# Kernel tuning notes

Hardware: AMD Instinct MI355X
Metric: run time of the kernel (lower is better)

## Reference

```python
import jax, jax.numpy as jnp
import numpy as np

N = 50000   # nodes
E = 800000  # edges
D = 64      # num_filters == hidden_channels
NG = 5      # num_gaussians (edge_attr width, unused by forward math)
NEG_SLOPE = 0.2


def setup_inputs() -> dict:
    key = jax.random.key(0)
    ks = jax.random.split(key, 16)
    s = 1.0 / np.sqrt(D)
    return {
        "x": jax.random.normal(ks[0], (N, D), dtype=jnp.float32),
        "edge_index": jax.random.randint(ks[1], (2, E), 0, N, dtype=jnp.int64),
        "edge_weight": jax.random.uniform(ks[2], (E,), dtype=jnp.float32),
        "edge_attr": jax.random.normal(ks[3], (E, NG), dtype=jnp.float32),
        "W0": jax.random.normal(ks[4], (D, D), dtype=jnp.float32) * s,
        "b0": jnp.zeros((D,), dtype=jnp.float32),
        "W1": jax.random.normal(ks[5], (D, D), dtype=jnp.float32) * s,
        "as1": jax.random.normal(ks[6], (D,), dtype=jnp.float32) * s,
        "ad1": jax.random.normal(ks[7], (D,), dtype=jnp.float32) * s,
        "b1": jnp.zeros((D,), dtype=jnp.float32),
        "W2": jax.random.normal(ks[8], (D, D), dtype=jnp.float32) * s,
        "as2": jax.random.normal(ks[9], (D,), dtype=jnp.float32) * s,
        "ad2": jax.random.normal(ks[10], (D,), dtype=jnp.float32) * s,
        "b2": jnp.zeros((D,), dtype=jnp.float32),
    }


def gat_layer(h, src, dst, W, a_src, a_dst, b):
    # PyG GATConv, heads=1, add_self_loops=False
    hx = h @ W  # [N, D]
    # per-node attention logits, gathered per edge (edge j->i: src=j, dst=i)
    alpha = (hx * a_src).sum(-1)[src] + (hx * a_dst).sum(-1)[dst]  # [E]
    alpha = jax.nn.leaky_relu(alpha, NEG_SLOPE)
    # segment softmax grouped by destination node
    m = jax.ops.segment_max(alpha, dst, num_segments=N)
    e = jnp.exp(alpha - m[dst])
    s = jax.ops.segment_sum(e, dst, num_segments=N)
    p = e / s[dst]  # [E]
    # scatter-add weighted source features
    out = jax.ops.segment_sum(hx[src] * p[:, None], dst, num_segments=N)
    return out + b


def reference(x, edge_index, edge_weight, edge_attr,
              W0, b0, W1, as1, ad1, b1, W2, as2, ad2, b2):
    # edge_weight / edge_attr are accepted but unused, as in the torch module
    src, dst = edge_index[0], edge_index[1]
    out = jax.nn.relu(x @ W0 + b0)
    out = out + jax.nn.relu(gat_layer(out, src, dst, W1, as1, ad1, b1))
    out = out + jax.nn.relu(gat_layer(out, src, dst, W2, as2, ad2, b2))
    return out
```

## Files before the change

### kernel.cpp

```cpp
#include <hip/hip_runtime.h>

#define DD 64
#define NEG_SLOPE 0.2f
#define HS 68
#define CAP 64
#define BSH 8
#define BN  256
#define NBMAX 256
#define NBLK 256
#define CAPB 6144
#define STAGE_CAP 6144
#define AMM_NODES 32
#define CWS 65

__device__ __forceinline__ unsigned short f2bf(float f)
{
    unsigned u = __float_as_uint(f);
    u += 0x7FFFu + ((u >> 16) & 1u);
    return (unsigned short)(u >> 16);
}
__device__ __forceinline__ float bf2f(unsigned short b)
{
    return __uint_as_float(((unsigned)b) << 16);
}

__device__ __forceinline__ int wave_incl_scan(int v, int lane)
{
#pragma unroll
    for (int off = 1; off < 64; off <<= 1) {
        int t = __shfl_up(v, off);
        if (lane >= off) v += t;
    }
    return v;
}

__device__ __forceinline__ void group_aggregate(
    const ushort4* __restrict__ hx, const int* __restrict__ col,
    const float* __restrict__ sarr, float adi, int beg, int deg, int fl,
    uint2* __restrict__ cw, float4& acc, float& s)
{
    s = 0.f;
    acc = float4{0.f, 0.f, 0.f, 0.f};

#define GATH(P) { float wv = __uint_as_float((P).y);                          \
                  ushort4 uu = hx[(P).x * 16 + fl];                           \
                  acc.x += wv * bf2f(uu.x); acc.y += wv * bf2f(uu.y);         \
                  acc.z += wv * bf2f(uu.z); acc.w += wv * bf2f(uu.w); }

    if (deg <= CAP) {
        int c0 = 0, c1 = 0, c2 = 0, c3 = 0;
        float w0 = 0.f, w1 = 0.f, w2 = 0.f, w3 = 0.f;
        if (fl < deg)      { c0 = col[beg + fl];      float a = sarr[c0] + adi; a = a > 0.f ? a : NEG_SLOPE * a; w0 = __expf(a); }
        if (fl + 16 < deg) { c1 = col[beg + fl + 16]; float a = sarr[c1] + adi; a = a > 0.f ? a : NEG_SLOPE * a; w1 = __expf(a); }
        if (fl + 32 < deg) { c2 = col[beg + fl + 32]; float a = sarr[c2] + adi; a = a > 0.f ? a : NEG_SLOPE * a; w2 = __expf(a); }
        if (fl + 48 < deg) { c3 = col[beg + fl + 48]; float a = sarr[c3] + adi; a = a > 0.f ? a : NEG_SLOPE * a; w3 = __expf(a); }
        s = (w0 + w1) + (w2 + w3);

        int degR = (deg + 7) & ~7;
        if (fl < degR)      { uint2 e; e.x = (unsigned)c0; e.y = __float_as_uint(w0); cw[fl] = e; }
        if (fl + 16 < degR) { uint2 e; e.x = (unsigned)c1; e.y = __float_as_uint(w1); cw[fl + 16] = e; }
        if (fl + 32 < degR) { uint2 e; e.x = (unsigned)c2; e.y = __float_as_uint(w2); cw[fl + 32] = e; }
        if (fl + 48 < degR) { uint2 e; e.x = (unsigned)c3; e.y = __float_as_uint(w3); cw[fl + 48] = e; }

        for (int i = 0; i < degR; i += 8) {
            uint2 p0 = cw[i],     p1 = cw[i + 1], p2 = cw[i + 2], p3 = cw[i + 3];
            uint2 p4 = cw[i + 4], p5 = cw[i + 5], p6 = cw[i + 6], p7 = cw[i + 7];
            GATH(p0); GATH(p1); GATH(p2); GATH(p3);
            GATH(p4); GATH(p5); GATH(p6); GATH(p7);
        }
    } else {
        for (int base = 0; base < deg; base += 16) {
            int i = base + fl;
            uint2 e; e.x = 0u; e.y = 0u;
            if (i < deg) {
                int c = col[beg + i];
                float a = sarr[c] + adi;
                a = a > 0.f ? a : NEG_SLOPE * a;
                float wv = __expf(a);
                e.x = (unsigned)c; e.y = __float_as_uint(wv);
                s += wv;
            }
            cw[fl] = e;
#pragma unroll
            for (int j = 0; j < 16; j += 8) {
                uint2 p0 = cw[j],     p1 = cw[j + 1], p2 = cw[j + 2], p3 = cw[j + 3];
                uint2 p4 = cw[j + 4], p5 = cw[j + 5], p6 = cw[j + 6], p7 = cw[j + 7];
                GATH(p0); GATH(p1); GATH(p2); GATH(p3);
                GATH(p4); GATH(p5); GATH(p6); GATH(p7);
            }
        }
    }
#pragma unroll
    for (int off = 8; off; off >>= 1) s += __shfl_xor(s, off);
#undef GATH
}

__global__ __launch_bounds__(512) void scatter_mm(
    const int4* __restrict__ dst4, const int4* __restrict__ src4,
    const int* __restrict__ dst, const int* __restrict__ src,
    int* __restrict__ gcur, int* __restrict__ ebuf,
    int NB, int E4, int E, int C4,
    const float* __restrict__ x, const float* __restrict__ W0,
    const float* __restrict__ b0, const float* __restrict__ W1,
    const float* __restrict__ a_src, const float* __restrict__ a_dst,
    float* __restrict__ h, ushort4* __restrict__ hxb4,
    float* __restrict__ sarr, float* __restrict__ darr, int n)
{
    __shared__ float smem[DD * DD + DD * HS];
    int tid = threadIdx.x;

    if (blockIdx.x < NBLK) {
        int* lh   = (int*)smem;
        int* lcur = lh + NBMAX;
        int k = blockIdx.x;
        for (int i = tid; i < NB; i += 512) lh[i] = 0;
        __syncthreads();
        int i0 = k * C4, i1 = min(i0 + C4, E4);
        for (int i = i0 + tid; i < i1; i += 512) {
            int4 d = dst4[i];
            atomicAdd(&lh[d.x >> BSH], 1);
            atomicAdd(&lh[d.y >> BSH], 1);
            atomicAdd(&lh[d.z >> BSH], 1);
            atomicAdd(&lh[d.w >> BSH], 1);
        }
        if (k == NBLK - 1) {
            for (int e = E4 * 4 + tid; e < E; e += 512)
                atomicAdd(&lh[dst[e] >> BSH], 1);
        }
        __syncthreads();
        for (int b = tid; b < NB; b += 512) {
            int c = lh[b];
            lcur[b] = b * CAPB + (c ? atomicAdd(&gcur[b], c) : 0);
        }
        __syncthreads();
        for (int i = i0 + tid; i < i1; i += 512) {
            int4 d = dst4[i];
            int4 s = src4[i];
            int b, p;
            b = d.x >> BSH; p = atomicAdd(&lcur[b], 1);
            if (p < b * CAPB + CAPB) ebuf[p] = ((d.x & (BN - 1)) << 24) | s.x;
            b = d.y >> BSH; p = atomicAdd(&lcur[b], 1);
            if (p < b * CAPB + CAPB) ebuf[p] = ((d.y & (BN - 1)) << 24) | s.y;
            b = d.z >> BSH; p = atomicAdd(&lcur[b], 1);
            if (p < b * CAPB + CAPB) ebuf[p] = ((d.z & (BN - 1)) << 24) | s.z;
            b = d.w >> BSH; p = atomicAdd(&lcur[b], 1);
            if (p < b * CAPB + CAPB) ebuf[p] = ((d.w & (BN - 1)) << 24) | s.w;
        }
        if (k == NBLK - 1) {
            for (int e = E4 * 4 + tid; e < E; e += 512) {
                int d = dst[e];
                int b = d >> BSH;
                int p = atomicAdd(&lcur[b], 1);
                if (p < b * CAPB + CAPB)
                    ebuf[p] = ((d & (BN - 1)) << 24) | src[e];
            }
        }
        return;
    }

    float* Wsh = smem;
    float* Hsh = smem + DD * DD;
    int fg = tid & 15, ng = tid >> 4;
    int tile0 = (blockIdx.x - NBLK) * 64;

    for (int i = tid * 4; i < DD * DD; i += 2048)
        *(float4*)&Wsh[i] = *(const float4*)&W0[i];
    for (int p = 0; p < 2; ++p) {
        int nl = p * 32 + ng, gn = tile0 + nl;
        if (gn < n)
            *(float4*)&Hsh[nl * HS + 4 * fg] = *(const float4*)&x[gn * DD + 4 * fg];
    }
    __syncthreads();

    float4 acc[2];
#pragma unroll
    for (int j = 0; j < 2; ++j) acc[j] = float4{0.f, 0.f, 0.f, 0.f};
#pragma unroll 8
    for (int k = 0; k < DD; ++k) {
        float4 w4 = *(float4*)&Wsh[k * DD + 4 * fg];
#pragma unroll
        for (int j = 0; j < 2; ++j) {
            float hv = Hsh[(2 * ng + j) * HS + k];
            acc[j].x += hv * w4.x; acc[j].y += hv * w4.y;
            acc[j].z += hv * w4.z; acc[j].w += hv * w4.w;
        }
    }

    float4 b4 = *(const float4*)&b0[4 * fg];
    float4 o[2];
#pragma unroll
    for (int j = 0; j < 2; ++j) {
        o[j].x = fmaxf(acc[j].x + b4.x, 0.f);
        o[j].y = fmaxf(acc[j].y + b4.y, 0.f);
        o[j].z = fmaxf(acc[j].z + b4.z, 0.f);
        o[j].w = fmaxf(acc[j].w + b4.w, 0.f);
        int gn = tile0 + 2 * ng + j;
        if (gn < n) *(float4*)&h[gn * DD + 4 * fg] = o[j];
    }
    __syncthreads();

#pragma unroll
    for (int j = 0; j < 2; ++j)
        *(float4*)&Hsh[(2 * ng + j) * HS + 4 * fg] = o[j];
    for (int i = tid * 4; i < DD * DD; i += 2048)
        *(float4*)&Wsh[i] = *(const float4*)&W1[i];
    __syncthreads();

#pragma unroll
    for (int j = 0; j < 2; ++j) acc[j] = float4{0.f, 0.f, 0.f, 0.f};
#pragma unroll 8
    for (int k = 0; k < DD; ++k) {
        float4 w4 = *(float4*)&Wsh[k * DD + 4 * fg];
#pragma unroll
        for (int j = 0; j < 2; ++j) {
            float hv = Hsh[(2 * ng + j) * HS + k];
            acc[j].x += hv * w4.x; acc[j].y += hv * w4.y;
            acc[j].z += hv * w4.z; acc[j].w += hv * w4.w;
        }
    }

    float4 as4 = *(const float4*)&a_src[4 * fg];
    float4 ad4 = *(const float4*)&a_dst[4 * fg];
#pragma unroll
    for (int j = 0; j < 2; ++j) {
        int gn = tile0 + 2 * ng + j;
        if (gn < n) {
            ushort4 hb;
            hb.x = f2bf(acc[j].x); hb.y = f2bf(acc[j].y);
            hb.z = f2bf(acc[j].z); hb.w = f2bf(acc[j].w);
            hxb4[gn * 16 + fg] = hb;
        }
        float ps = acc[j].x * as4.x + acc[j].y * as4.y + acc[j].z * as4.z + acc[j].w * as4.w;
        float pd = acc[j].x * ad4.x + acc[j].y * ad4.y + acc[j].z * ad4.z + acc[j].w * ad4.w;
#pragma unroll
        for (int off = 8; off; off >>= 1) {
            ps += __shfl_xor(ps, off);
            pd += __shfl_xor(pd, off);
        }
        if (fg == 0 && gn < n) { sarr[gn] = ps; darr[gn] = pd; }
    }
}

__global__ __launch_bounds__(512) void group_build(
    const int* __restrict__ ebuf, const int* __restrict__ gcur,
    int* __restrict__ row_beg, int* __restrict__ degarr,
    int* __restrict__ col, int N)
{
    __shared__ int lcnt[BN];
    __shared__ int loff[BN];
    __shared__ int lcur[BN];
    __shared__ int wsum[4];
    __shared__ int stage[STAGE_CAP];
    int b = blockIdx.x, tid = threadIdx.x;
    int e0 = b * CAPB;
    int total = min(gcur[b], CAPB);
    int e1 = e0 + total;
    if (tid < BN) { lcnt[tid] = 0; lcur[tid] = 0; }
    __syncthreads();
    for (int e = e0 + tid; e < e1; e += 512)
        atomicAdd(&lcnt[((unsigned)ebuf[e]) >> 24], 1);
    __syncthreads();
    int lane = tid & 63, w = tid >> 6;
    int v = (tid < BN) ? lcnt[tid] : 0;
    int incl = wave_incl_scan(v, lane);
    if (tid < BN && lane == 63) wsum[w] = incl;
    __syncthreads();
    if (tid < BN) {
        int wo = 0;
        for (int i = 0; i < w; ++i) wo += wsum[i];
        int excl = wo + incl - v;
        loff[tid] = excl;
        int node = b * BN + tid;
        if (node < N) { row_beg[node] = e0 + excl; degarr[node] = v; }
    }
    __syncthreads();
    for (int e = e0 + tid; e < e1; e += 512) {
        int p = ebuf[e];
        int dl = ((unsigned)p) >> 24;
        int r = atomicAdd(&lcur[dl], 1);
        stage[loff[dl] + r] = p & 0xFFFFFF;
    }
    __syncthreads();
    for (int i = tid; i < total; i += 512)
        col[e0 + i] = stage[i];
}

__global__ __launch_bounds__(512) void agg_mm(
    const ushort4* __restrict__ hxA, const int* __restrict__ row_beg,
    const int* __restrict__ degarr, const int* __restrict__ col,
    const float* __restrict__ sA, const float* __restrict__ dA,
    const float* __restrict__ bias,
    float* __restrict__ h, const float* __restrict__ W,
    const float* __restrict__ a_src, const float* __restrict__ a_dst,
    ushort4* __restrict__ hxB, float* __restrict__ sB, float* __restrict__ dB,
    int n)
{
    __shared__ float Wsh[DD * DD];
    __shared__ uint2 cwbuf[AMM_NODES][CWS];
    float* Hsh = (float*)&cwbuf[0][0];

    int tid = threadIdx.x;
    int w = tid >> 6, lane = tid & 63, grp = lane >> 4, fl = lane & 15;
    int nl = 4 * w + grp;
    int tile0 = blockIdx.x * AMM_NODES;
    int v = tile0 + nl;
    bool alive = v < n;

    for (int i = tid * 4; i < DD * DD; i += 2048)
        *(float4*)&Wsh[i] = *(const float4*)&W[i];

    int beg = 0, deg = 0;
    float adi = 0.f;
    if (alive) {
        beg = row_beg[v];
        deg = degarr[v];
        adi = dA[v];
    }

    float4 acc; float s;
    group_aggregate(hxA, col, sA, adi, beg, deg, fl, &cwbuf[nl][0], acc, s);

    float4 resid = float4{0.f, 0.f, 0.f, 0.f};
    {
        float inv = (s > 0.f) ? 1.f / s : 0.f;
        float4 b4 = ((const float4*)bias)[fl];
        float4 o;
        o.x = fmaxf(acc.x * inv + b4.x, 0.f);
        o.y = fmaxf(acc.y * inv + b4.y, 0.f);
        o.z = fmaxf(acc.z * inv + b4.z, 0.f);
        o.w = fmaxf(acc.w * inv + b4.w, 0.f);
        if (alive) {
            float4* hp = (float4*)&h[v * DD + 4 * fl];
            float4 cur = *hp;
            cur.x += o.x; cur.y += o.y; cur.z += o.z; cur.w += o.w;
            *hp = cur;
            resid = cur;
        }
    }
    __syncthreads();
    *(float4*)&Hsh[nl * HS + 4 * fl] = resid;
    __syncthreads();

    int nl2 = tid >> 4;
    int fg = tid & 15;
    float4 acc2 = float4{0.f, 0.f, 0.f, 0.f};
#pragma unroll 8
    for (int k = 0; k < DD; ++k) {
        float4 w4 = *(float4*)&Wsh[k * DD + 4 * fg];
        float hv = Hsh[nl2 * HS + k];
        acc2.x += hv * w4.x; acc2.y += hv * w4.y;
        acc2.z += hv * w4.z; acc2.w += hv * w4.w;
    }
    int gn = tile0 + nl2;
    float4 as4 = *(const float4*)&a_src[4 * fg];
    float4 ad4 = *(const float4*)&a_dst[4 * fg];
    if (gn < n) {
        ushort4 hb;
        hb.x = f2bf(acc2.x); hb.y = f2bf(acc2.y);
        hb.z = f2bf(acc2.z); hb.w = f2bf(acc2.w);
        hxB[gn * 16 + fg] = hb;
    }
    float ps = acc2.x * as4.x + acc2.y * as4.y + acc2.z * as4.z + acc2.w * as4.w;
    float pd = acc2.x * ad4.x + acc2.y * ad4.y + acc2.z * ad4.z + acc2.w * ad4.w;
#pragma unroll
    for (int off = 8; off; off >>= 1) {
        ps += __shfl_xor(ps, off);
        pd += __shfl_xor(pd, off);
    }
    if (fg == 0 && gn < n) { sB[gn] = ps; dB[gn] = pd; }
}

__global__ __launch_bounds__(512) void aggregate(
    const ushort4* __restrict__ hxb4, const int* __restrict__ row_beg,
    const int* __restrict__ degarr, const int* __restrict__ col,
    const float* __restrict__ sarr, const float* __restrict__ darr,
    const float* __restrict__ bias, float* __restrict__ h, int n)
{
    __shared__ uint2 cwbuf[AMM_NODES][CWS];
    int tid = threadIdx.x;
    int w = tid >> 6, lane = tid & 63, grp = lane >> 4, fl = lane & 15;
    int nl = 4 * w + grp;
    int v = blockIdx.x * AMM_NODES + nl;
    bool alive = v < n;

    int beg = 0, deg = 0;
    float adi = 0.f;
    if (alive) {
        beg = row_beg[v];
        deg = degarr[v];
        adi = darr[v];
    }

    float4 acc; float s;
    group_aggregate(hxb4, col, sarr, adi, beg, deg, fl, &cwbuf[nl][0], acc, s);

    if (alive) {
        float inv = (s > 0.f) ? 1.f / s : 0.f;
        float4 b4 = ((const float4*)bias)[fl];
        float4 o;
        o.x = fmaxf(acc.x * inv + b4.x, 0.f);
        o.y = fmaxf(acc.y * inv + b4.y, 0.f);
        o.z = fmaxf(acc.z * inv + b4.z, 0.f);
        o.w = fmaxf(acc.w * inv + b4.w, 0.f);
        float4* hp = (float4*)&h[v * DD + 4 * fl];
        float4 cur = *hp;
        cur.x += o.x; cur.y += o.y; cur.z += o.z; cur.w += o.w;
        *hp = cur;
    }
}

extern "C" void kernel_launch(void* const* d_in, const int* in_sizes, int n_in,
                              void* d_out, int out_size, void* d_ws, size_t ws_size,
                              hipStream_t stream)
{
    const float* x  = (const float*)d_in[0];
    const int*   ei = (const int*)d_in[1];
    const float* W0 = (const float*)d_in[4];
    const float* b0 = (const float*)d_in[5];
    const float* W1 = (const float*)d_in[6];
    const float* as1= (const float*)d_in[7];
    const float* ad1= (const float*)d_in[8];
    const float* b1 = (const float*)d_in[9];
    const float* W2 = (const float*)d_in[10];
    const float* as2= (const float*)d_in[11];
    const float* ad2= (const float*)d_in[12];
    const float* b2 = (const float*)d_in[13];

    int N = in_sizes[0] / DD;
    int E = in_sizes[1] / 2;
    int E4 = E >> 2;
    int C4 = (E4 + NBLK - 1) / NBLK;
    int NB = (N + BN - 1) >> BSH;
    float* h = (float*)d_out;

    ushort4* hxA  = (ushort4*)d_ws;
    ushort4* hxB  = hxA + (size_t)N * 16;
    float* sA     = (float*)(hxB + (size_t)N * 16);
    float* dA     = sA + N;
    float* sB     = dA + N;
    float* dB     = sB + N;
    int*   row_beg= (int*)(dB + N);
    int*   degarr = row_beg + N;
    int*   gcur   = degarr + N;
    int*   ebuf   = gcur + NB;
    int*   colb   = ebuf + (size_t)NB * CAPB;

    const int* src = ei;
    const int* dst = ei + E;
    const int4* dst4 = (const int4*)dst;
    const int4* src4 = (const int4*)src;

    int tiles   = (N + 63) / 64;
    int ntiles  = (N + AMM_NODES - 1) / AMM_NODES;

    hipMemsetAsync(gcur, 0, NB * sizeof(int), stream);
    scatter_mm<<<NBLK + tiles, 512, 0, stream>>>(
        dst4, src4, dst, src, gcur, ebuf, NB, E4, E, C4,
        x, W0, b0, W1, as1, ad1, h, hxA, sA, dA, N);
    group_build<<<NB, 512, 0, stream>>>(ebuf, gcur, row_beg, degarr, colb, N);
    agg_mm<<<ntiles, 512, 0, stream>>>(hxA, row_beg, degarr, colb, sA, dA, b1,
                                       h, W2, as2, ad2, hxB, sB, dB, N);
    aggregate<<<ntiles, 512, 0, stream>>>(hxB, row_beg, degarr, colb,
                                          sB, dB, b2, h, N);
}
```

Measured before the change: 178.4 us.

## Fuse group_build into scatter_mm via per-bucket completion counters and late claiming

Removes the separate group_build launch. Each scatter block bumps a per-bucket counter with release semantics once its edges are written. Every block, at its end, claims any bucket whose counter shows all scatter blocks are done and builds that bucket's CSR segment in shared memory. This saves a kernel launch and lets CSR building overlap with the trailing matmul tiles. The cost is extra atomics and a smaller shared stage aliased onto smem, and buckets may be unevenly assigned to whichever blocks finish late.

```diff
diff --git a/kernel.cpp b/kernel.cpp
--- a/kernel.cpp
+++ b/kernel.cpp
@@ -95,10 +95,52 @@
 #undef GATH
 }
 
-__global__ __launch_bounds__(512) void scatter_mm(
+__device__ __forceinline__ void build_bucket(
+    int b, const int* __restrict__ ebuf, const int* __restrict__ gcur,
+    int* __restrict__ row_beg, int* __restrict__ degarr, int* __restrict__ col,
+    int N, int* stage, int* lcnt, int* loff, int* lcur, int* wsum)
+{
+    int tid = threadIdx.x;
+    int e0 = b * CAPB;
+    int total = min(gcur[b], CAPB);
+    int e1 = e0 + total;
+    if (tid < BN) { lcnt[tid] = 0; lcur[tid] = 0; }
+    __syncthreads();
+    for (int e = e0 + tid; e < e1; e += 512)
+        atomicAdd(&lcnt[((unsigned)ebuf[e]) >> 24], 1);
+    __syncthreads();
+    int lane = tid & 63, w = tid >> 6;
+    int v = (tid < BN) ? lcnt[tid] : 0;
+    int incl = wave_incl_scan(v, lane);
+    if (tid < BN && lane == 63) wsum[w] = incl;
+    __syncthreads();
+    if (tid < BN) {
+        int wo = 0;
+        for (int i = 0; i < w; ++i) wo += wsum[i];
+        int excl = wo + incl - v;
+        loff[tid] = excl;
+        int node = b * BN + tid;
+        if (node < N) { row_beg[node] = e0 + excl; degarr[node] = v; }
+    }
+    __syncthreads();
+    for (int e = e0 + tid; e < e1; e += 512) {
+        int p = ebuf[e];
+        int dl = ((unsigned)p) >> 24;
+        int r = atomicAdd(&lcur[dl], 1);
+        stage[loff[dl] + r] = p & 0xFFFFFF;
+    }
+    __syncthreads();
+    for (int i = tid; i < total; i += 512)
+        col[e0 + i] = stage[i];
+    __syncthreads();
+}
+
+__global__ __launch_bounds__(512) void scatter_mm_gb(
     const int4* __restrict__ dst4, const int4* __restrict__ src4,
     const int* __restrict__ dst, const int* __restrict__ src,
-    int* __restrict__ gcur, int* __restrict__ ebuf,
+    int* __restrict__ gcur, int* __restrict__ cnt, int* __restrict__ bstate,
+    int* __restrict__ ebuf,
+    int* __restrict__ row_beg, int* __restrict__ degarr, int* __restrict__ colb,
     int NB, int E4, int E, int C4,
     const float* __restrict__ x, const float* __restrict__ W0,
     const float* __restrict__ b0, const float* __restrict__ W1,
@@ -107,6 +149,8 @@
     float* __restrict__ sarr, float* __restrict__ darr, int n)
 {
     __shared__ float smem[DD * DD + DD * HS];
+    __shared__ int blist[NBMAX];
+    __shared__ int nclaim;
     int tid = threadIdx.x;
 
     if (blockIdx.x < NBLK) {
@@ -155,134 +199,116 @@
                     ebuf[p] = ((d & (BN - 1)) << 24) | src[e];
             }
         }
-        return;
-    }
-
-    float* Wsh = smem;
-    float* Hsh = smem + DD * DD;
-    int fg = tid & 15, ng = tid >> 4;
-    int tile0 = (blockIdx.x - NBLK) * 64;
-
-    for (int i = tid * 4; i < DD * DD; i += 2048)
-        *(float4*)&Wsh[i] = *(const float4*)&W0[i];
-    for (int p = 0; p < 2; ++p) {
-        int nl = p * 32 + ng, gn = tile0 + nl;
-        if (gn < n)
-            *(float4*)&Hsh[nl * HS + 4 * fg] = *(const float4*)&x[gn * DD + 4 * fg];
-    }
-    __syncthreads();
-
-    float4 acc[2];
-#pragma unroll
-    for (int j = 0; j < 2; ++j) acc[j] = float4{0.f, 0.f, 0.f, 0.f};
+        __threadfence();
+        __syncthreads();
+        for (int b = tid; b < NB; b += 512)
+            __hip_atomic_fetch_add(&cnt[b], 1, __ATOMIC_RELEASE,
+                                   __HIP_MEMORY_SCOPE_AGENT);
+    } else {
+        float* Wsh = smem;
+        float* Hsh = smem + DD * DD;
+        int fg = tid & 15, ng = tid >> 4;
+        int tile0 = (blockIdx.x - NBLK) * 64;
+
+        for (int i = tid * 4; i < DD * DD; i += 2048)
+            *(float4*)&Wsh[i] = *(const float4*)&W0[i];
+        for (int p = 0; p < 2; ++p) {
+            int nl = p * 32 + ng, gn = tile0 + nl;
+            if (gn < n)
+                *(float4*)&Hsh[nl * HS + 4 * fg] = *(const float4*)&x[gn * DD + 4 * fg];
+        }
+        __syncthreads();
+
+        float4 acc[2];
+#pragma unroll
+        for (int j = 0; j < 2; ++j) acc[j] = float4{0.f, 0.f, 0.f, 0.f};
 #pragma unroll 8
-    for (int k = 0; k < DD; ++k) {
-        float4 w4 = *(float4*)&Wsh[k * DD + 4 * fg];
+        for (int k = 0; k < DD; ++k) {
+            float4 w4 = *(float4*)&Wsh[k * DD + 4 * fg];
+#pragma unroll
+            for (int j = 0; j < 2; ++j) {
+                float hv = Hsh[(2 * ng + j) * HS + k];
+                acc[j].x += hv * w4.x; acc[j].y += hv * w4.y;
+                acc[j].z += hv * w4.z; acc[j].w += hv * w4.w;
+            }
+        }
+
+        float4 b4 = *(const float4*)&b0[4 * fg];
+        float4 o[2];
 #pragma unroll
         for (int j = 0; j < 2; ++j) {
-            float hv = Hsh[(2 * ng + j) * HS + k];
-            acc[j].x += hv * w4.x; acc[j].y += hv * w4.y;
-            acc[j].z += hv * w4.z; acc[j].w += hv * w4.w;
-        }
-    }
-
-    float4 b4 = *(const float4*)&b0[4 * fg];
-    float4 o[2];
-#pragma unroll
-    for (int j = 0; j < 2; ++j) {
-        o[j].x = fmaxf(acc[j].x + b4.x, 0.f);
-        o[j].y = fmaxf(acc[j].y + b4.y, 0.f);
-        o[j].z = fmaxf(acc[j].z + b4.z, 0.f);
-        o[j].w = fmaxf(acc[j].w + b4.w, 0.f);
-        int gn = tile0 + 2 * ng + j;
-        if (gn < n) *(float4*)&h[gn * DD + 4 * fg] = o[j];
-    }
-    __syncthreads();
-
-#pragma unroll
-    for (int j = 0; j < 2; ++j)
-        *(float4*)&Hsh[(2 * ng + j) * HS + 4 * fg] = o[j];
-    for (int i = tid * 4; i < DD * DD; i += 2048)
-        *(float4*)&Wsh[i] = *(const float4*)&W1[i];
-    __syncthreads();
-
-#pragma unroll
-    for (int j = 0; j < 2; ++j) acc[j] = float4{0.f, 0.f, 0.f, 0.f};
+            o[j].x = fmaxf(acc[j].x + b4.x, 0.f);
+            o[j].y = fmaxf(acc[j].y + b4.y, 0.f);
+            o[j].z = fmaxf(acc[j].z + b4.z, 0.f);
+            o[j].w = fmaxf(acc[j].w + b4.w, 0.f);
+            int gn = tile0 + 2 * ng + j;
+            if (gn < n) *(float4*)&h[gn * DD + 4 * fg] = o[j];
+        }
+        __syncthreads();
+
+#pragma unroll
+        for (int j = 0; j < 2; ++j)
+            *(float4*)&Hsh[(2 * ng + j) * HS + 4 * fg] = o[j];
+        for (int i = tid * 4; i < DD * DD; i += 2048)
+            *(float4*)&Wsh[i] = *(const float4*)&W1[i];
+        __syncthreads();
+
+#pragma unroll
+        for (int j = 0; j < 2; ++j) acc[j] = float4{0.f, 0.f, 0.f, 0.f};
 #pragma unroll 8
-    for (int k = 0; k < DD; ++k) {
-        float4 w4 = *(float4*)&Wsh[k * DD + 4 * fg];
+        for (int k = 0; k < DD; ++k) {
+            float4 w4 = *(float4*)&Wsh[k * DD + 4 * fg];
+#pragma unroll
+            for (int j = 0; j < 2; ++j) {
+                float hv = Hsh[(2 * ng + j) * HS + k];
+                acc[j].x += hv * w4.x; acc[j].y += hv * w4.y;
+                acc[j].z += hv * w4.z; acc[j].w += hv * w4.w;
+            }
+        }
+
+        float4 as4 = *(const float4*)&a_src[4 * fg];
+        float4 ad4 = *(const float4*)&a_dst[4 * fg];
 #pragma unroll
         for (int j = 0; j < 2; ++j) {
-            float hv = Hsh[(2 * ng + j) * HS + k];
-            acc[j].x += hv * w4.x; acc[j].y += hv * w4.y;
-            acc[j].z += hv * w4.z; acc[j].w += hv * w4.w;
-        }
-    }
-
-    float4 as4 = *(const float4*)&a_src[4 * fg];
-    float4 ad4 = *(const float4*)&a_dst[4 * fg];
-#pragma unroll
-    for (int j = 0; j < 2; ++j) {
-        int gn = tile0 + 2 * ng + j;
-        if (gn < n) {
-            ushort4 hb;
-            hb.x = f2bf(acc[j].x); hb.y = f2bf(acc[j].y);
-            hb.z = f2bf(acc[j].z); hb.w = f2bf(acc[j].w);
-            hxb4[gn * 16 + fg] = hb;
-        }
-        float ps = acc[j].x * as4.x + acc[j].y * as4.y + acc[j].z * as4.z + acc[j].w * as4.w;
-        float pd = acc[j].x * ad4.x + acc[j].y * ad4.y + acc[j].z * ad4.z + acc[j].w * ad4.w;
-#pragma unroll
-        for (int off = 8; off; off >>= 1) {
-            ps += __shfl_xor(ps, off);
-            pd += __shfl_xor(pd, off);
-        }
-        if (fg == 0 && gn < n) { sarr[gn] = ps; darr[gn] = pd; }
-    }
-}
-
-__global__ __launch_bounds__(512) void group_build(
-    const int* __restrict__ ebuf, const int* __restrict__ gcur,
-    int* __restrict__ row_beg, int* __restrict__ degarr,
-    int* __restrict__ col, int N)
-{
-    __shared__ int lcnt[BN];
-    __shared__ int loff[BN];
-    __shared__ int lcur[BN];
-    __shared__ int wsum[4];
-    __shared__ int stage[STAGE_CAP];
-    int b = blockIdx.x, tid = threadIdx.x;
-    int e0 = b * CAPB;
-    int total = min(gcur[b], CAPB);
-    int e1 = e0 + total;
-    if (tid < BN) { lcnt[tid] = 0; lcur[tid] = 0; }
-    __syncthreads();
-    for (int e = e0 + tid; e < e1; e += 512)
-        atomicAdd(&lcnt[((unsigned)ebuf[e]) >> 24], 1);
-    __syncthreads();
-    int lane = tid & 63, w = tid >> 6;
-    int v = (tid < BN) ? lcnt[tid] : 0;
-    int incl = wave_incl_scan(v, lane);
-    if (tid < BN && lane == 63) wsum[w] = incl;
-    __syncthreads();
-    if (tid < BN) {
-        int wo = 0;
-        for (int i = 0; i < w; ++i) wo += wsum[i];
-        int excl = wo + incl - v;
-        loff[tid] = excl;
-        int node = b * BN + tid;
-        if (node < N) { row_beg[node] = e0 + excl; degarr[node] = v; }
-    }
-    __syncthreads();
-    for (int e = e0 + tid; e < e1; e += 512) {
-        int p = ebuf[e];
-        int dl = ((unsigned)p) >> 24;
-        int r = atomicAdd(&lcur[dl], 1);
-        stage[loff[dl] + r] = p & 0xFFFFFF;
-    }
-    __syncthreads();
-    for (int i = tid; i < total; i += 512)
-        col[e0 + i] = stage[i];
+            int gn = tile0 + 2 * ng + j;
+            if (gn < n) {
+                ushort4 hb;
+                hb.x = f2bf(acc[j].x); hb.y = f2bf(acc[j].y);
+                hb.z = f2bf(acc[j].z); hb.w = f2bf(acc[j].w);
+                hxb4[gn * 16 + fg] = hb;
+            }
+            float ps = acc[j].x * as4.x + acc[j].y * as4.y + acc[j].z * as4.z + acc[j].w * as4.w;
+            float pd = acc[j].x * ad4.x + acc[j].y * ad4.y + acc[j].z * ad4.z + acc[j].w * ad4.w;
+#pragma unroll
+            for (int off = 8; off; off >>= 1) {
+                ps += __shfl_xor(ps, off);
+                pd += __shfl_xor(pd, off);
+            }
+            if (fg == 0 && gn < n) { sarr[gn] = ps; darr[gn] = pd; }
+        }
+    }
+
+    __syncthreads();
+    if (tid == 0) nclaim = 0;
+    __syncthreads();
+    if (tid < NB) {
+        if (__hip_atomic_load(&cnt[tid], __ATOMIC_ACQUIRE,
+                              __HIP_MEMORY_SCOPE_AGENT) == NBLK &&
+            atomicCAS(&bstate[tid], 0, 1) == 0)
+            blist[atomicAdd(&nclaim, 1)] = tid;
+    }
+    __syncthreads();
+    int nc = nclaim;
+    if (nc > 0) {
+        int* stage = (int*)smem;
+        int* lcnt  = stage + STAGE_CAP;
+        int* loff  = lcnt + BN;
+        int* lcur  = loff + BN;
+        int* wsum  = lcur + BN;
+        for (int i = 0; i < nc; ++i)
+            build_bucket(blist[i], ebuf, gcur, row_beg, degarr, colb, n,
+                         stage, lcnt, loff, lcur, wsum);
+    }
 }
 
 __global__ __launch_bounds__(512) void agg_mm(
@@ -442,7 +468,9 @@
     int*   row_beg= (int*)(dB + N);
     int*   degarr = row_beg + N;
     int*   gcur   = degarr + N;
-    int*   ebuf   = gcur + NB;
+    int*   cnt    = gcur + NB;
+    int*   bstate = cnt + NB;
+    int*   ebuf   = bstate + NB;
     int*   colb   = ebuf + (size_t)NB * CAPB;
 
     const int* src = ei;
@@ -453,11 +481,11 @@
     int tiles   = (N + 63) / 64;
     int ntiles  = (N + AMM_NODES - 1) / AMM_NODES;
 
-    hipMemsetAsync(gcur, 0, NB * sizeof(int), stream);
-    scatter_mm<<<NBLK + tiles, 512, 0, stream>>>(
-        dst4, src4, dst, src, gcur, ebuf, NB, E4, E, C4,
+    hipMemsetAsync(gcur, 0, 3 * NB * sizeof(int), stream);
+    scatter_mm_gb<<<NBLK + tiles, 512, 0, stream>>>(
+        dst4, src4, dst, src, gcur, cnt, bstate, ebuf,
+        row_beg, degarr, colb, NB, E4, E, C4,
         x, W0, b0, W1, as1, ad1, h, hxA, sA, dA, N);
-    group_build<<<NB, 512, 0, stream>>>(ebuf, gcur, row_beg, degarr, colb, N);
     agg_mm<<<ntiles, 512, 0, stream>>>(hxA, row_beg, degarr, colb, sA, dA, b1,
                                        h, W2, as2, ad2, hxB, sB, dB, N);
     aggregate<<<ntiles, 512, 0, stream>>>(hxB, row_beg, degarr, colb,
```

Result: slower. 560.8 us (+214.3%).
